# Performance work log

Hardware: AMD Instinct MI355X
Metric: run time of the kernel (lower is better)

The kernel has to match this reference:

```python
import jax, jax.numpy as jnp
import numpy as np

B, S, D, H, E, K = 2, 1024, 512, 2048, 8, 2

def setup_inputs() -> dict:
    key = jax.random.key(0)
    k1, k2, k3, k4, k5 = jax.random.split(key, 5)
    std = 0.02
    return {
        "x": jax.random.normal(k1, (B, S, D), dtype=jnp.float32),
        "indices": jax.random.randint(k2, (B, S, K), 0, E, dtype=jnp.int32),
        "weights": jax.random.uniform(k3, (B, S, K), dtype=jnp.float32),
        "keys": std * jax.random.normal(k4, (D, E, H), dtype=jnp.float32),
        "key_bias": jnp.zeros((E, H), dtype=jnp.float32),
        "values": std * jax.random.normal(k5, (H, E, D), dtype=jnp.float32),
        "value_bias": jnp.zeros((E, D), dtype=jnp.float32),
    }

def reference(x, indices, weights, keys, key_bias, values, value_bias):
    # Faithful to FeedForward.process_by_indices: for each token, run the FFN of
    # each of its top-k experts and sum results weighted by routing weights.
    # Expressed as dense all-expert compute + sparse one-hot combine (identical math).
    b, s, d = x.shape
    k = indices.shape[-1]
    e = keys.shape[1]
    xt = x.reshape(-1, d)                      # [T, D]
    idx = indices.reshape(-1, k)               # [T, K]
    w = weights.reshape(-1, k)                 # [T, K]
    # per-expert FFN for all tokens: hidden [T, E, H]
    hidden = jax.nn.gelu(jnp.einsum('td,deh->teh', xt, keys) + key_bias)
    out_e = jnp.einsum('teh,heo->teo', hidden, values) + value_bias  # [T, E, D]
    # combine matrix: sum_k weight_k * onehot(expert_k)  -> [T, E]
    comb = jnp.sum(jax.nn.one_hot(idx, e, dtype=xt.dtype) * w[..., None], axis=1)
    out = jnp.einsum('teo,te->to', out_e, comb)  # [T, D]
    return out.reshape(b, s, d)
```

## Files before the change

kernel.cpp:

```cpp
#include <hip/hip_runtime.h>
#include <hip/hip_bf16.h>

#define TB   2048
#define DD   512
#define HH   2048
#define EE   8
#define TK   4096

typedef __attribute__((ext_vector_type(8))) __bf16 bf16x8;
typedef __attribute__((ext_vector_type(4))) float  f32x4;
typedef __attribute__((ext_vector_type(4))) unsigned int u32x4;

#define KSPLIT1 4

__device__ __forceinline__ unsigned short f2bf(float f) {
  return __builtin_bit_cast(unsigned short, (__bf16)f);
}

__global__ void route_kernel(const int* __restrict__ idx, const float* __restrict__ wts,
                             int* cnt, int* offs, int* rowt, int* pos, float* wrow) {
  __shared__ int s_cnt[EE], s_off[EE], s_fill[EE];
  int tid = threadIdx.x;
  if (tid < EE) s_cnt[tid] = 0;
  __syncthreads();
  for (int i = tid; i < TK; i += 256) atomicAdd(&s_cnt[idx[i]], 1);
  __syncthreads();
  if (tid == 0) {
    int acc = 0;
    for (int e = 0; e < EE; ++e) { s_off[e] = acc; acc += s_cnt[e]; s_fill[e] = s_off[e]; }
  }
  __syncthreads();
  for (int i = tid; i < TK; i += 256) {
    int e = idx[i];
    int r = atomicAdd(&s_fill[e], 1);
    rowt[r] = i;
    pos[i]  = r;
    wrow[r] = wts[i];
  }
  if (tid < EE) { cnt[tid] = s_cnt[tid]; offs[tid] = s_off[tid]; }
}

__global__ __launch_bounds__(256) void prep_kernel(
    const float* __restrict__ x, const int* __restrict__ rowt, unsigned short* __restrict__ Xg,
    const float* __restrict__ keys, unsigned short* __restrict__ kT,
    float* __restrict__ out) {
  int bid = blockIdx.x;
  int tid = threadIdx.x;
  if (bid < 1024) {
    ((float4*)out)[bid * 256 + tid] = float4{0.f, 0.f, 0.f, 0.f};
    int i = bid * 256 + tid;
    int r = i >> 6;
    int c = i & 63;
    int t = rowt[r] >> 1;
    const float4* src = (const float4*)(x + (size_t)t * DD + c * 8);
    float4 a = src[0], b = src[1];
    unsigned short res[8];
    res[0]=f2bf(a.x); res[1]=f2bf(a.y); res[2]=f2bf(a.z); res[3]=f2bf(a.w);
    res[4]=f2bf(b.x); res[5]=f2bf(b.y); res[6]=f2bf(b.z); res[7]=f2bf(b.w);
    *(uint4*)(Xg + (size_t)r * DD + c * 8) = *(uint4*)res;
    return;
  }
  __shared__ unsigned short tt[64][66];
  int rel = bid - 1024; int e = rel >> 8; int rem = rel & 255;
  int k0 = (rem >> 5) * 64, n0 = (rem & 31) * 64;
  #pragma unroll
  for (int it = 0; it < 4; ++it) {
    int idx = tid + it * 256;
    int r  = idx >> 4;
    int c4 = idx & 15;
    float4 v = *(const float4*)(keys + (size_t)(k0 + r) * (EE * HH) + (size_t)e * HH + n0 + c4 * 4);
    unsigned short q[4] = {f2bf(v.x), f2bf(v.y), f2bf(v.z), f2bf(v.w)};
    *(uint2*)&tt[r][c4 * 4] = *(uint2*)q;
  }
  __syncthreads();
  #pragma unroll
  for (int it = 0; it < 2; ++it) {
    int idx = tid + it * 256;
    int n  = idx >> 3;
    int kc = (idx & 7) * 8;
    unsigned short q[8];
    #pragma unroll
    for (int i = 0; i < 8; ++i) q[i] = tt[kc + i][n];
    *(uint4*)(kT + ((size_t)e * HH + n0 + n) * DD + k0 + kc) = *(uint4*)q;
  }
}

__device__ __forceinline__ void vt_transpose(unsigned short* smem, const float* __restrict__ values,
                                             unsigned short* __restrict__ vT, int bid, int tid) {
  int e = bid & 7, rem = bid >> 3;
  int k0 = (rem >> 3) * 64;
  int n0 = (rem & 7) * 64;
  unsigned short (*tt)[66] = (unsigned short(*)[66])smem;
  #pragma unroll
  for (int it = 0; it < 4; ++it) {
    int idx = tid + it * 256;
    int r = idx >> 4, c4 = idx & 15;
    const f32x4* sp = (const f32x4*)(values + (size_t)(k0 + r) * (EE * DD) + (size_t)e * DD + n0 + c4 * 4);
    f32x4 v = __builtin_nontemporal_load(sp);
    unsigned short q[4] = {f2bf(v.x), f2bf(v.y), f2bf(v.z), f2bf(v.w)};
    *(uint2*)&tt[r][c4 * 4] = *(uint2*)q;
  }
  __syncthreads();
  #pragma unroll
  for (int it = 0; it < 2; ++it) {
    int idx = tid + it * 256;
    int n = idx >> 3;
    int kc = (idx & 7) * 8;
    unsigned short q[8];
    #pragma unroll
    for (int i = 0; i < 8; ++i) q[i] = tt[kc + i][n];
    __builtin_nontemporal_store(*(u32x4*)q, (u32x4*)(vT + ((size_t)e * DD + n0 + n) * HH + k0 + kc));
  }
}

template<int ROWS>
__device__ __forceinline__ void stage_swz(const char* src, int src_stride,
                                          unsigned short* lds, int wave, int lane) {
  constexpr int PW = ROWS * 128 / 1024 / 4;
  #pragma unroll
  for (int j = 0; j < PW; ++j) {
    int base = (wave * PW + j) * 1024;
    int o = base + lane * 16;
    int row  = o >> 7;
    int slot = (o >> 4) & 7;
    const char* g = src + (size_t)row * src_stride + ((slot ^ (row & 7)) << 4);
    __builtin_amdgcn_global_load_lds(
        (const __attribute__((address_space(1))) unsigned*)g,
        (__attribute__((address_space(3))) unsigned*)((char*)lds + base), 16, 0, 0);
  }
}

template<int BM, int BN, int PASS, int KSPLIT>
__device__ __forceinline__ void ffn_gemm_body(
    int bid, unsigned short* smem,
    const unsigned short* __restrict__ Aall, const unsigned short* __restrict__ Bw,
    const float* __restrict__ bias,
    const int* __restrict__ cnt, const int* __restrict__ offs,
    const float* __restrict__ wrow, const int* __restrict__ rowt,
    unsigned short* __restrict__ outA, float* __restrict__ fout)
{
  constexpr int KDIM = (PASS == 0) ? DD : HH;
  constexpr int NDIM = (PASS == 0) ? HH : DD;
  constexpr int KLEN = KDIM / KSPLIT;
  constexpr int NT   = KLEN / 64;
  constexpr int NX   = NDIM / BN;
  constexpr int NY   = TK / BM;
  constexpr int PER_E = NY * NX * KSPLIT;
  constexpr int NWG  = EE * PER_E;
  constexpr int WM = BM / 2, WN = BN / 2;
  constexpr int FM = WM / 16, FN = WN / 16;

  int swz = (bid & 7) * (NWG / 8) + (bid >> 3);
  int e   = swz / PER_E;
  int rem = swz % PER_E;
  int mblk = rem / (NX * KSPLIT);
  int r2   = rem % (NX * KSPLIT);
  int xblk = r2 / KSPLIT;
  int ks   = r2 % KSPLIT;

  const int n_e = cnt[e];
  if (mblk * BM >= n_e) return;
  const int off_e = offs[e];
  const int bn = xblk * BN;

  unsigned short* Sb0 = smem;
  unsigned short* Sb1 = smem + (BM + BN) * 64;

  const int tid  = threadIdx.x;
  const int lane = tid & 63;
  const int wave = tid >> 6;
  const int wm = wave >> 1, wn = wave & 1;
  const int lr = lane & 15;
  const int kg = lane >> 4;

  const char* Ab = (const char*)(Aall + (size_t)(off_e + mblk * BM) * KDIM + ks * KLEN);
  const char* Bb = (const char*)(Bw + ((size_t)e * NDIM + bn) * KDIM + ks * KLEN);

  f32x4 acc[FM][FN] = {};

  auto STAGE = [&](unsigned short* buf, int kt) {
    stage_swz<BM>(Ab + kt * 128, KDIM * 2, buf, wave, lane);
    stage_swz<BN>(Bb + kt * 128, KDIM * 2, buf + BM * 64, wave, lane);
  };
  auto COMPUTE = [&](const unsigned short* buf) {
    const char* As = (const char*)buf;
    const char* Bs = (const char*)(buf + BM * 64);
    #pragma unroll
    for (int kss = 0; kss < 2; ++kss) {
      bf16x8 af[FM], bfv[FN];
      #pragma unroll
      for (int fm = 0; fm < FM; ++fm) {
        int r = wm * WM + fm * 16 + lr;
        int sl = (kss * 4 + kg) ^ (r & 7);
        af[fm] = *(const bf16x8*)(As + r * 128 + (sl << 4));
      }
      #pragma unroll
      for (int fn = 0; fn < FN; ++fn) {
        int r = wn * WN + fn * 16 + lr;
        int sl = (kss * 4 + kg) ^ (r & 7);
        bfv[fn] = *(const bf16x8*)(Bs + r * 128 + (sl << 4));
      }
      #pragma unroll
      for (int fm = 0; fm < FM; ++fm)
        #pragma unroll
        for (int fn = 0; fn < FN; ++fn)
          acc[fm][fn] = __builtin_amdgcn_mfma_f32_16x16x32_bf16(af[fm], bfv[fn], acc[fm][fn], 0, 0, 0);
    }
  };

  STAGE(Sb0, 0);
  __syncthreads();
  #pragma unroll 2
  for (int kt = 0; kt < NT; kt += 2) {
    if (kt + 1 < NT) STAGE(Sb1, kt + 1);
    COMPUTE(Sb0);
    __syncthreads();
    if (kt + 2 < NT) STAGE(Sb0, kt + 2);
    COMPUTE(Sb1);
    __syncthreads();
  }

  const int rq = kg * 4;
  #pragma unroll
  for (int fm = 0; fm < FM; ++fm) {
    int row0 = mblk * BM + wm * WM + fm * 16 + rq;
    #pragma unroll
    for (int fn = 0; fn < FN; ++fn) {
      int col = bn + wn * WN + fn * 16 + lr;
      float bs = (PASS == 0 || ks == 0) ? bias[e * NDIM + col] : 0.f;
      #pragma unroll
      for (int i = 0; i < 4; ++i) {
        int rl = row0 + i;
        if (rl < n_e) {
          float v = acc[fm][fn][i] + bs;
          if (PASS == 0) {
            float u = 0.7978845608f * (v + 0.044715f * v * v * v);
            float g = v / (1.f + __expf(-2.f * u));
            outA[(size_t)(off_e + rl) * HH + col] = f2bf(g);
          } else {
            float w = wrow[off_e + rl];
            int tkn = rowt[off_e + rl] >> 1;
            atomicAdd(fout + (size_t)tkn * DD + col, v * w);
          }
        }
      }
    }
  }
}

__global__ __launch_bounds__(256, 5) void ffn_gemm_p0(
    const unsigned short* __restrict__ Aall, const unsigned short* __restrict__ Bw,
    const float* __restrict__ bias, const int* __restrict__ cnt, const int* __restrict__ offs,
    const float* __restrict__ wrow, unsigned short* __restrict__ outA,
    const float* __restrict__ values, unsigned short* __restrict__ vT) {
  __shared__ __align__(1024) unsigned short smem[2 * (64 + 64) * 64];
  int bid = blockIdx.x;
  if (bid < 2048) { vt_transpose(smem, values, vT, bid, threadIdx.x); return; }
  ffn_gemm_body<64, 64, 0, 1>(bid - 2048, smem, Aall, Bw, bias, cnt, offs, wrow,
                              nullptr, outA, nullptr);
}
__global__ __launch_bounds__(256, 5) void ffn_gemm_p1(
    const unsigned short* __restrict__ Aall, const unsigned short* __restrict__ Bw,
    const float* __restrict__ bias, const int* __restrict__ cnt, const int* __restrict__ offs,
    const float* __restrict__ wrow, const int* __restrict__ rowt, float* __restrict__ fout) {
  __shared__ __align__(1024) unsigned short smem[2 * (64 + 64) * 64];
  ffn_gemm_body<64, 64, 1, KSPLIT1>(blockIdx.x, smem, Aall, Bw, bias, cnt, offs, wrow,
                                    rowt, nullptr, fout);
}

extern "C" void kernel_launch(void* const* d_in, const int* in_sizes, int n_in,
                              void* d_out, int out_size, void* d_ws, size_t ws_size,
                              hipStream_t stream) {
  const float* x          = (const float*)d_in[0];
  const int*   indices    = (const int*)d_in[1];
  const float* weights    = (const float*)d_in[2];
  const float* keys       = (const float*)d_in[3];
  const float* key_bias   = (const float*)d_in[4];
  const float* values     = (const float*)d_in[5];
  const float* value_bias = (const float*)d_in[6];
  float* out = (float*)d_out;

  char* ws = (char*)d_ws;
  int*   cnt  = (int*)(ws);
  int*   offs = (int*)(ws + 256);
  int*   rowt = (int*)(ws + 512);
  int*   pos  = (int*)(ws + 512 + 4 * TK);
  float* wrow = (float*)(ws + 512 + 8 * TK);
  unsigned short* Xg      = (unsigned short*)(ws + (64u << 10));
  unsigned short* hid     = (unsigned short*)(ws + (8u  << 20));
  unsigned short* kT      = (unsigned short*)(ws + (26u << 20));
  unsigned short* vT      = (unsigned short*)(ws + (43u << 20));

  route_kernel<<<1, 256, 0, stream>>>(indices, weights, cnt, offs, rowt, pos, wrow);
  prep_kernel<<<3072, 256, 0, stream>>>(x, rowt, Xg, keys, kT, out);

  ffn_gemm_p0<<<2048 + EE * (TK/64) * (HH/64), 256, 0, stream>>>(
      Xg, kT, key_bias, cnt, offs, wrow, hid, values, vT);
  ffn_gemm_p1<<<EE * (TK/64) * (DD/64) * KSPLIT1, 256, 0, stream>>>(
      hid, vT, value_bias, cnt, offs, wrow, rowt, out);
}
```

Measured before the change: 102.1 us.

## Replace atomic scatter-add with bf16 partial buffers and a gather combine kernel

The second GEMM now writes each weighted expert-row result as bf16 into a per-k-split contribution buffer instead of doing fp32 atomicAdd into the output. A new combine kernel gathers each token's two routed rows across splits and writes the output directly, so the output zeroing in prep is dropped. The k-split of pass 1 is reduced from 4 to 2, and the vT transpose store becomes a regular store. This removes atomic contention and the memset, at the cost of an extra launch, an extra round trip through memory, and bf16 rounding of the partial sums. The contribution buffer reuses the kT region, which is safe only because kT is dead once pass 0 finishes.

```diff
diff --git a/kernel.cpp b/kernel.cpp
--- a/kernel.cpp
+++ b/kernel.cpp
@@ -11,10 +11,14 @@
 typedef __attribute__((ext_vector_type(4))) float  f32x4;
 typedef __attribute__((ext_vector_type(4))) unsigned int u32x4;
 
-#define KSPLIT1 4
+#define CONTRIB_ELEMS ((size_t)TK * DD)
+#define KSPLIT1 2
 
 __device__ __forceinline__ unsigned short f2bf(float f) {
   return __builtin_bit_cast(unsigned short, (__bf16)f);
+}
+__device__ __forceinline__ float bf2f(unsigned short h) {
+  union { unsigned u; float f; } c; c.u = (unsigned)h << 16; return c.f;
 }
 
 __global__ void route_kernel(const int* __restrict__ idx, const float* __restrict__ wts,
@@ -42,12 +46,10 @@
 
 __global__ __launch_bounds__(256) void prep_kernel(
     const float* __restrict__ x, const int* __restrict__ rowt, unsigned short* __restrict__ Xg,
-    const float* __restrict__ keys, unsigned short* __restrict__ kT,
-    float* __restrict__ out) {
+    const float* __restrict__ keys, unsigned short* __restrict__ kT) {
   int bid = blockIdx.x;
   int tid = threadIdx.x;
   if (bid < 1024) {
-    ((float4*)out)[bid * 256 + tid] = float4{0.f, 0.f, 0.f, 0.f};
     int i = bid * 256 + tid;
     int r = i >> 6;
     int c = i & 63;
@@ -109,7 +111,7 @@
     unsigned short q[8];
     #pragma unroll
     for (int i = 0; i < 8; ++i) q[i] = tt[kc + i][n];
-    __builtin_nontemporal_store(*(u32x4*)q, (u32x4*)(vT + ((size_t)e * DD + n0 + n) * HH + k0 + kc));
+    *(uint4*)(vT + ((size_t)e * DD + n0 + n) * HH + k0 + kc) = *(uint4*)q;
   }
 }
 
@@ -136,8 +138,8 @@
     const unsigned short* __restrict__ Aall, const unsigned short* __restrict__ Bw,
     const float* __restrict__ bias,
     const int* __restrict__ cnt, const int* __restrict__ offs,
-    const float* __restrict__ wrow, const int* __restrict__ rowt,
-    unsigned short* __restrict__ outA, float* __restrict__ fout)
+    const float* __restrict__ wrow,
+    unsigned short* __restrict__ outA, unsigned short* __restrict__ outB)
 {
   constexpr int KDIM = (PASS == 0) ? DD : HH;
   constexpr int NDIM = (PASS == 0) ? HH : DD;
@@ -239,8 +241,7 @@
             outA[(size_t)(off_e + rl) * HH + col] = f2bf(g);
           } else {
             float w = wrow[off_e + rl];
-            int tkn = rowt[off_e + rl] >> 1;
-            atomicAdd(fout + (size_t)tkn * DD + col, v * w);
+            outB[ks * CONTRIB_ELEMS + (size_t)(off_e + rl) * DD + col] = f2bf(v * w);
           }
         }
       }
@@ -257,15 +258,37 @@
   int bid = blockIdx.x;
   if (bid < 2048) { vt_transpose(smem, values, vT, bid, threadIdx.x); return; }
   ffn_gemm_body<64, 64, 0, 1>(bid - 2048, smem, Aall, Bw, bias, cnt, offs, wrow,
-                              nullptr, outA, nullptr);
+                              outA, nullptr);
 }
 __global__ __launch_bounds__(256, 5) void ffn_gemm_p1(
     const unsigned short* __restrict__ Aall, const unsigned short* __restrict__ Bw,
     const float* __restrict__ bias, const int* __restrict__ cnt, const int* __restrict__ offs,
-    const float* __restrict__ wrow, const int* __restrict__ rowt, float* __restrict__ fout) {
+    const float* __restrict__ wrow, unsigned short* __restrict__ outB) {
   __shared__ __align__(1024) unsigned short smem[2 * (64 + 64) * 64];
   ffn_gemm_body<64, 64, 1, KSPLIT1>(blockIdx.x, smem, Aall, Bw, bias, cnt, offs, wrow,
-                                    rowt, nullptr, fout);
+                                    nullptr, outB);
+}
+
+__global__ void combine(const unsigned short* __restrict__ contrib, const int* __restrict__ pos,
+                        float* __restrict__ out) {
+  int i = blockIdx.x * blockDim.x + threadIdx.x;
+  int t = i >> 6;
+  int c = i & 63;
+  int r0 = pos[t * 2], r1 = pos[t * 2 + 1];
+  float o[8] = {0,0,0,0,0,0,0,0};
+  #pragma unroll
+  for (int p = 0; p < KSPLIT1; ++p) {
+    const unsigned short* base = contrib + (size_t)p * CONTRIB_ELEMS;
+    union { uint4 q; unsigned short h[8]; } a, b;
+    a.q = *(const uint4*)(base + (size_t)r0 * DD + c * 8);
+    b.q = *(const uint4*)(base + (size_t)r1 * DD + c * 8);
+    #pragma unroll
+    for (int j = 0; j < 8; ++j)
+      o[j] += bf2f(a.h[j]) + bf2f(b.h[j]);
+  }
+  float* dst = out + (size_t)t * DD + c * 8;
+  *(float4*)dst       = *(float4*)&o[0];
+  *(float4*)(dst + 4) = *(float4*)&o[4];
 }
 
 extern "C" void kernel_launch(void* const* d_in, const int* in_sizes, int n_in,
@@ -290,12 +313,14 @@
   unsigned short* hid     = (unsigned short*)(ws + (8u  << 20));
   unsigned short* kT      = (unsigned short*)(ws + (26u << 20));
   unsigned short* vT      = (unsigned short*)(ws + (43u << 20));
+  unsigned short* contrib = (unsigned short*)(ws + (26u << 20));
 
   route_kernel<<<1, 256, 0, stream>>>(indices, weights, cnt, offs, rowt, pos, wrow);
-  prep_kernel<<<3072, 256, 0, stream>>>(x, rowt, Xg, keys, kT, out);
+  prep_kernel<<<3072, 256, 0, stream>>>(x, rowt, Xg, keys, kT);
 
   ffn_gemm_p0<<<2048 + EE * (TK/64) * (HH/64), 256, 0, stream>>>(
       Xg, kT, key_bias, cnt, offs, wrow, hid, values, vT);
   ffn_gemm_p1<<<EE * (TK/64) * (DD/64) * KSPLIT1, 256, 0, stream>>>(
-      hid, vT, value_bias, cnt, offs, wrow, rowt, out);
-}
+      hid, vT, value_bias, cnt, offs, wrow, contrib);
+  combine<<<(TB * 64) / 256, 256, 0, stream>>>(contrib, pos, out);
+}
```

After: 82.25 us, median of 2. 19.4% less time.
